# Kernel tuning notes

Hardware: AMD Instinct MI355X
Metric: run time of the kernel (lower is better)

## Reference

```python
import jax, jax.numpy as jnp
import numpy as np


def setup_inputs() -> dict:
    key = jax.random.key(0)
    B, F1, F2 = 1024, 32, 16
    X = jax.random.normal(key, (B, F1, F2), dtype=jnp.float32)
    return {"X": X}


def reference(X) -> jnp.ndarray:
    # Flatten feature dims: [B, ele]
    B = X.shape[0]
    ele = X.shape[1] * X.shape[2]
    x = X.reshape(B, ele)
    # Upper-triangular pair indices (i outer, j inner, j >= i) — matches the
    # torch double loop's row-major enumeration of pairs.
    ii, jj = jnp.triu_indices(ele)  # each [ele*(ele+1)/2]
    # Pairwise products via gather + elementwise mul (avoids full [B,ele,ele] outer)
    out = x[:, ii] * x[:, jj]  # [B, npairs]
    return out[:, :, None]  # [B, npairs, 1]
```

## Files before the change

kernel.cpp:

```cpp
#include <hip/hip_runtime.h>
#include <hip/hip_bf16.h>


#define ELE 512
#define NPAIRS 131328
#define GROUPS 32832
#define BLOCKS_PER_BATCH 16
#define GROUPS_PER_BLOCK 2052

__device__ __forceinline__ int row_off(int i) {
    return (i * (1025 - i)) >> 1;
}

__global__ __launch_bounds__(256) void pairmul4_kernel(
    const float* __restrict__ X, float* __restrict__ out) {
    const int bid = blockIdx.x;
    const int b = bid / BLOCKS_PER_BATCH;
    const int c = bid % BLOCKS_PER_BATCH;

    const float* __restrict__ xb = X + (size_t)b * ELE;
    float4* __restrict__ ob = (float4*)(out + (size_t)b * NPAIRS);

    const int glo = c * GROUPS_PER_BLOCK;
    const int ghi = glo + GROUPS_PER_BLOCK;

    for (int g = glo + (int)threadIdx.x; g < ghi; g += 256) {
        const int p = g << 2;
        float s = sqrtf((float)(1050625 - 8 * p));
        int i = (int)((1025.0f - s) * 0.5f);
        i = min(max(i, 0), 511);
        int o0 = row_off(i);
        int o1 = o0 + (ELE - i);
        while (o1 <= p) { ++i; o0 = o1; o1 += (ELE - i); }
        while (o0 > p)  { --i; o1 = o0; o0 -= (ELE - i); }

        float4 v;
        if (p + 3 < o1) {
            const float xi = xb[i];
            const int j = i + (p - o0);
            v.x = xi * xb[j];
            v.y = xi * xb[j + 1];
            v.z = xi * xb[j + 2];
            v.w = xi * xb[j + 3];
        } else {
            float r[4];
            int ii = i, oo0 = o0, oo1 = o1;
            #pragma unroll
            for (int t = 0; t < 4; ++t) {
                const int pt = p + t;
                while (oo1 <= pt) { ++ii; oo0 = oo1; oo1 += (ELE - ii); }
                r[t] = xb[ii] * xb[ii + (pt - oo0)];
            }
            v = make_float4(r[0], r[1], r[2], r[3]);
        }
        ob[g] = v;
    }
}

extern "C" void kernel_launch(void* const* d_in, const int* in_sizes, int n_in,
                              void* d_out, int out_size, void* d_ws, size_t ws_size,
                              hipStream_t stream) {
    const float* X = (const float*)d_in[0];
    float* out = (float*)d_out;

    const int B = in_sizes[0] / ELE;
    dim3 grid(B * BLOCKS_PER_BATCH);
    dim3 block(256);
    pairmul4_kernel<<<grid, block, 0, stream>>>(X, out);
}
```

Baseline: 135.6 us.

## Stage row in shared memory with shifted copies, nontemporal stores, fewer blocks

Each block loads its 512-float batch row into LDS and builds three shifted copies, so an unaligned 4-wide window can be read as one aligned 16-byte LDS load instead of four scattered global loads. Output writes use nontemporal stores to avoid polluting cache with the large streaming output. Blocks per batch are halved, so each block does twice the work and the LDS setup is amortised, though the grid has fewer blocks. The kernel is store-bound (~537MB written), so the gains may be small.

```diff
diff --git a/kernel.cpp b/kernel.cpp
--- a/kernel.cpp
+++ b/kernel.cpp
@@ -5,55 +5,64 @@
 #define ELE 512
 #define NPAIRS 131328
 #define GROUPS 32832
-#define BLOCKS_PER_BATCH 16
-#define GROUPS_PER_BLOCK 2052
+#define BPB 8
+#define GPB 4104
 
-__device__ __forceinline__ int row_off(int i) {
-    return (i * (1025 - i)) >> 1;
-}
+typedef float f4 __attribute__((ext_vector_type(4)));
 
 __global__ __launch_bounds__(256) void pairmul4_kernel(
     const float* __restrict__ X, float* __restrict__ out) {
     const int bid = blockIdx.x;
-    const int b = bid / BLOCKS_PER_BATCH;
-    const int c = bid % BLOCKS_PER_BATCH;
+    const int b = bid >> 3;
+    const int c = bid & 7;
 
     const float* __restrict__ xb = X + (size_t)b * ELE;
-    float4* __restrict__ ob = (float4*)(out + (size_t)b * NPAIRS);
+    f4* __restrict__ ob = (f4*)(out + (size_t)b * NPAIRS);
 
-    const int glo = c * GROUPS_PER_BLOCK;
-    const int ghi = glo + GROUPS_PER_BLOCK;
+    __shared__ __align__(16) float xs4[4][516];
+    const int t = threadIdx.x;
+    xs4[0][t]       = xb[t];
+    xs4[0][t + 256] = xb[t + 256];
+    __syncthreads();
+    #pragma unroll
+    for (int cc = 1; cc < 4; ++cc) {
+        xs4[cc][t]       = xs4[0][t + cc];
+        xs4[cc][t + 256] = (t + 256 + cc < ELE) ? xs4[0][t + 256 + cc] : 0.0f;
+    }
+    __syncthreads();
 
-    for (int g = glo + (int)threadIdx.x; g < ghi; g += 256) {
+    const int glo = c * GPB;
+    const int ghi = glo + GPB;
+
+    for (int g = glo + t; g < ghi; g += 256) {
         const int p = g << 2;
         float s = sqrtf((float)(1050625 - 8 * p));
         int i = (int)((1025.0f - s) * 0.5f);
         i = min(max(i, 0), 511);
-        int o0 = row_off(i);
+        int o0 = (i * (1025 - i)) >> 1;
         int o1 = o0 + (ELE - i);
         while (o1 <= p) { ++i; o0 = o1; o1 += (ELE - i); }
         while (o0 > p)  { --i; o1 = o0; o0 -= (ELE - i); }
 
-        float4 v;
+        f4 v;
         if (p + 3 < o1) {
-            const float xi = xb[i];
+            const float xi = xs4[0][i];
             const int j = i + (p - o0);
-            v.x = xi * xb[j];
-            v.y = xi * xb[j + 1];
-            v.z = xi * xb[j + 2];
-            v.w = xi * xb[j + 3];
+            const f4* yc = (const f4*)(&xs4[j & 3][0]);
+            const f4 xv = yc[j >> 2];
+            v = xi * xv;
         } else {
             float r[4];
             int ii = i, oo0 = o0, oo1 = o1;
             #pragma unroll
-            for (int t = 0; t < 4; ++t) {
-                const int pt = p + t;
+            for (int e = 0; e < 4; ++e) {
+                const int pt = p + e;
                 while (oo1 <= pt) { ++ii; oo0 = oo1; oo1 += (ELE - ii); }
-                r[t] = xb[ii] * xb[ii + (pt - oo0)];
+                r[e] = xs4[0][ii] * xs4[0][ii + (pt - oo0)];
             }
-            v = make_float4(r[0], r[1], r[2], r[3]);
+            v.x = r[0]; v.y = r[1]; v.z = r[2]; v.w = r[3];
         }
-        ob[g] = v;
+        __builtin_nontemporal_store(v, &ob[g]);
     }
 }
 
@@ -64,7 +73,7 @@
     float* out = (float*)d_out;
 
     const int B = in_sizes[0] / ELE;
-    dim3 grid(B * BLOCKS_PER_BATCH);
+    dim3 grid(B * BPB);
     dim3 block(256);
     pairmul4_kernel<<<grid, block, 0, stream>>>(X, out);
 }
```

Measured after the change: 112.1 us. 1.21x faster.
